# Kernel tuning notes

Measured on AMD Instinct MI355X. Metric: run time of the kernel, lower is better.

Reference implementation:

```python
import math
import jax, jax.numpy as jnp
import numpy as np

N_HEADS = 8

def setup_inputs() -> dict:
    key = jax.random.key(0)
    qkv = jax.random.normal(key, (4, 3 * N_HEADS * 64, 2048), dtype=jnp.float32)
    return {"qkv": qkv}

def reference(qkv) -> jnp.ndarray:
    bs, width, length = qkv.shape
    assert width % (3 * N_HEADS) == 0
    ch = width // (3 * N_HEADS)
    q, k, v = jnp.split(qkv, 3, axis=1)            # each [N, H*C, T]
    scale = 1.0 / math.sqrt(math.sqrt(ch))
    qh = (q * scale).reshape(bs * N_HEADS, ch, length)  # [BH, C, T]
    kh = (k * scale).reshape(bs * N_HEADS, ch, length)
    vh = v.reshape(bs * N_HEADS, ch, length)
    weight = jnp.einsum('bct,bcs->bts', qh, kh)    # [BH, T, T]
    weight = jax.nn.softmax(weight.astype(jnp.float32), axis=-1).astype(weight.dtype)
    a = jnp.einsum('bts,bcs->bct', weight, vh)     # [BH, C, T]
    return a.reshape(bs, -1, length)
```

## Files before the change

kernel.cpp:

```cpp
#include <hip/hip_runtime.h>
#include <math.h>

#define T_LEN 2048
#define CH 64
#define NH 8
#define STILE 64
#define TTILE 128
#define WT 32
#define NIT (T_LEN / STILE)
#define CSK 68
#define CS 72
#define QS 132

#define QSCALE 0.180336880972948929f

typedef __attribute__((ext_vector_type(4))) float  f32x4;
typedef __attribute__((ext_vector_type(8))) __bf16 bf16x8;
typedef __attribute__((ext_vector_type(4))) __bf16 bf16x4;

union SMem {
  float qstage[CH * QS];
  struct {
    __bf16 k_hi[2][STILE * CSK];
    __bf16 v_s [2][CH * CS];
    __bf16 p_s [4 * WT * CS];
  } loop;
};

#define MFMA(A, B, C) __builtin_amdgcn_mfma_f32_16x16x32_bf16((A), (B), (C), 0, 0, 0)

__device__ __forceinline__ void load_k(const float* kp, int s0, int tid, float2 (&kreg)[2][4]) {
#pragma unroll
  for (int rr = 0; rr < 2; ++rr) {
    int fidx = rr * 256 + tid;
    int cq  = fidx >> 5;
    int sp2 = fidx & 31;
    const float* kc = kp + (size_t)(4 * cq) * T_LEN + s0 + 2 * sp2;
#pragma unroll
    for (int r = 0; r < 4; ++r)
      kreg[rr][r] = *(const float2*)(kc + (size_t)r * T_LEN);
  }
}

__device__ __forceinline__ void store_k(__bf16* kh, int tid, const float2 (&kreg)[2][4]) {
#pragma unroll
  for (int rr = 0; rr < 2; ++rr) {
    int fidx = rr * 256 + tid;
    int cq  = fidx >> 5;
    int sp2 = fidx & 31;
    bf16x4 w0 = {(__bf16)kreg[rr][0].x, (__bf16)kreg[rr][1].x,
                 (__bf16)kreg[rr][2].x, (__bf16)kreg[rr][3].x};
    bf16x4 w1 = {(__bf16)kreg[rr][0].y, (__bf16)kreg[rr][1].y,
                 (__bf16)kreg[rr][2].y, (__bf16)kreg[rr][3].y};
    *(bf16x4*)&kh[(2 * sp2 + 0) * CSK + 4 * cq] = w0;
    *(bf16x4*)&kh[(2 * sp2 + 1) * CSK + 4 * cq] = w1;
  }
}

__device__ __forceinline__ void load_v(const float* vp, int s0, int tid, f32x4 (&vreg)[4]) {
#pragma unroll
  for (int rr = 0; rr < 4; ++rr) {
    int fidx = rr * 256 + tid;
    int c  = fidx >> 4;
    int s4 = (fidx & 15) << 2;
    vreg[rr] = *(const f32x4*)(vp + (size_t)c * T_LEN + s0 + s4);
  }
}

__device__ __forceinline__ void store_v(__bf16* vs, int tid, const f32x4 (&vreg)[4]) {
#pragma unroll
  for (int rr = 0; rr < 4; ++rr) {
    int fidx = rr * 256 + tid;
    int c  = fidx >> 4;
    int s4 = (fidx & 15) << 2;
    bf16x4 vv = {(__bf16)vreg[rr].x, (__bf16)vreg[rr].y,
                 (__bf16)vreg[rr].z, (__bf16)vreg[rr].w};
    *(bf16x4*)&vs[c * CS + s4] = vv;
  }
}

__global__ __launch_bounds__(256, 2)
void qkv_attn_mfma(const float* __restrict__ qkv, float* __restrict__ out) {
  __shared__ SMem sm;
  const int tid  = threadIdx.x;
  const int lane = tid & 63;
  const int wave = tid >> 6;
  const int tn   = lane & 15;
  const int quad = lane >> 4;

  const int ttile = blockIdx.x;
  const int bh    = blockIdx.y;
  const int b = bh >> 3, h = bh & 7;
  const size_t base = (size_t)b * (3 * NH * CH) * T_LEN;
  const float* qp = qkv + base + (size_t)(CH * h) * T_LEN;
  const float* kp = qkv + base + (size_t)(CH * (NH + h)) * T_LEN;
  const float* vp = qkv + base + (size_t)(CH * (2 * NH + h)) * T_LEN;
  const int t0 = ttile * TTILE;

#pragma unroll
  for (int rr = 0; rr < 8; ++rr) {
    int fidx = rr * 256 + tid;
    int c  = fidx >> 5;
    int t4 = (fidx & 31) << 2;
    f32x4 q4 = *(const f32x4*)(qp + (size_t)c * T_LEN + t0 + t4);
    *(f32x4*)&sm.qstage[c * QS + t4] = q4;
  }
  __syncthreads();

  bf16x8 qh[2][2], ql[2][2];
#pragma unroll
  for (int nb = 0; nb < 2; ++nb)
#pragma unroll
    for (int kb = 0; kb < 2; ++kb) {
      int tloc = wave * WT + nb * 16 + tn;
      bf16x8 H, L;
#pragma unroll
      for (int j = 0; j < 8; ++j) {
        float qv = sm.qstage[(kb * 32 + quad * 8 + j) * QS + tloc] * QSCALE;
        __bf16 hv = (__bf16)qv;
        H[j] = hv;
        L[j] = (__bf16)(qv - (float)hv);
      }
      qh[nb][kb] = H;
      ql[nb][kb] = L;
    }
  __syncthreads();

  f32x4 acc[4][2];
  float l_part[2] = {0.f, 0.f};
#pragma unroll
  for (int mb = 0; mb < 4; ++mb)
#pragma unroll
    for (int nb = 0; nb < 2; ++nb)
      acc[mb][nb] = (f32x4){0.f, 0.f, 0.f, 0.f};

  float2 kreg[2][4];
  f32x4  vreg[4];
  load_k(kp, 0, tid, kreg);
  load_v(vp, 0, tid, vreg);
  store_k(sm.loop.k_hi[0], tid, kreg);
  store_v(sm.loop.v_s[0], tid, vreg);
  __syncthreads();

  for (int it = 0; it < NIT; ++it) {
    const int cur = it & 1;
    const bool more = (it + 1 < NIT);
    const int snext = (it + 1) * STILE;

    if (more) {
      load_k(kp, snext, tid, kreg);
      load_v(vp, snext, tid, vreg);
    }

    const __bf16* kh = sm.loop.k_hi[cur];
    const __bf16* vs = sm.loop.v_s[cur];

    f32x4 d[4][2];
#pragma unroll
    for (int mb = 0; mb < 4; ++mb) {
      const int srow = (mb * 16 + tn) * CSK + quad * 8;
      bf16x4 a00 = *(const bf16x4*)&kh[srow];
      bf16x4 a01 = *(const bf16x4*)&kh[srow + 4];
      bf16x4 a10 = *(const bf16x4*)&kh[srow + 32];
      bf16x4 a11 = *(const bf16x4*)&kh[srow + 36];
      bf16x8 ah0 = __builtin_shufflevector(a00, a01, 0, 1, 2, 3, 4, 5, 6, 7);
      bf16x8 ah1 = __builtin_shufflevector(a10, a11, 0, 1, 2, 3, 4, 5, 6, 7);
#pragma unroll
      for (int nb = 0; nb < 2; ++nb) {
        f32x4 acc_d = (f32x4){0.f, 0.f, 0.f, 0.f};
        acc_d = MFMA(ah0, qh[nb][0], acc_d);
        acc_d = MFMA(ah0, ql[nb][0], acc_d);
        acc_d = MFMA(ah1, qh[nb][1], acc_d);
        acc_d = MFMA(ah1, ql[nb][1], acc_d);
        d[mb][nb] = acc_d;
      }
    }

#pragma unroll
    for (int nb = 0; nb < 2; ++nb) {
      float rs = 0.f;
#pragma unroll
      for (int mb = 0; mb < 4; ++mb)
#pragma unroll
        for (int r = 0; r < 4; ++r) {
          float e = __builtin_amdgcn_exp2f(d[mb][nb][r]);
          d[mb][nb][r] = e;
          rs += e;
        }
      l_part[nb] += rs;
    }

    bf16x8 av[4][2];
#pragma unroll
    for (int mb = 0; mb < 4; ++mb) {
      const int crow = (mb * 16 + tn) * CS + quad * 8;
      av[mb][0] = *(const bf16x8*)&vs[crow];
      av[mb][1] = *(const bf16x8*)&vs[crow + 32];
    }

    __bf16* pw = &sm.loop.p_s[wave * (WT * CS)];
#pragma unroll
    for (int nb = 0; nb < 2; ++nb)
#pragma unroll
      for (int mb = 0; mb < 4; ++mb) {
        f32x4 pv4 = d[mb][nb];
        bf16x4 pb = {(__bf16)pv4.x, (__bf16)pv4.y, (__bf16)pv4.z, (__bf16)pv4.w};
        *(bf16x4*)&pw[(nb * 16 + tn) * CS + mb * 16 + quad * 4] = pb;
      }

    asm volatile("" ::: "memory");

    bf16x8 bp[2][2];
#pragma unroll
    for (int nb = 0; nb < 2; ++nb)
#pragma unroll
      for (int kb = 0; kb < 2; ++kb)
        bp[nb][kb] = *(const bf16x8*)&pw[(nb * 16 + tn) * CS + kb * 32 + quad * 8];

#pragma unroll
    for (int mb = 0; mb < 4; ++mb)
#pragma unroll
      for (int nb = 0; nb < 2; ++nb) {
        acc[mb][nb] = MFMA(av[mb][0], bp[nb][0], acc[mb][nb]);
        acc[mb][nb] = MFMA(av[mb][1], bp[nb][1], acc[mb][nb]);
      }

    if (more) {
      store_k(sm.loop.k_hi[cur ^ 1], tid, kreg);
      store_v(sm.loop.v_s[cur ^ 1], tid, vreg);
    }
    __syncthreads();
  }

  float* op = out + (size_t)bh * CH * T_LEN;
#pragma unroll
  for (int nb = 0; nb < 2; ++nb) {
    float l = l_part[nb];
    l += __shfl_xor(l, 16, 64);
    l += __shfl_xor(l, 32, 64);
    float inv_l = 1.0f / l;
    int t = t0 + wave * WT + nb * 16 + tn;
#pragma unroll
    for (int mb = 0; mb < 4; ++mb) {
      f32x4 o = acc[mb][nb] * inv_l;
      int c = mb * 16 + quad * 4;
      op[(size_t)(c + 0) * T_LEN + t] = o.x;
      op[(size_t)(c + 1) * T_LEN + t] = o.y;
      op[(size_t)(c + 2) * T_LEN + t] = o.z;
      op[(size_t)(c + 3) * T_LEN + t] = o.w;
    }
  }
}

extern "C" void kernel_launch(void* const* d_in, const int* in_sizes, int n_in,
                              void* d_out, int out_size, void* d_ws, size_t ws_size,
                              hipStream_t stream) {
  const float* qkv = (const float*)d_in[0];
  float* out = (float*)d_out;
  dim3 grid(T_LEN / TTILE, 32);
  qkv_attn_mfma<<<grid, 256, 0, stream>>>(qkv, out);
}
```

Baseline: 133.9 us.

## Load V fragments directly from global into MFMA registers, drop V LDS staging

Each wave now reads its own V operand fragments straight from global memory in MFMA layout and converts them to bf16 in registers, instead of staging a shared V tile through LDS. This removes the LDS writes and reads for V and frees shared memory. The P stride is widened to cut bank conflicts. The trade-off is that all four waves redundantly load the same V tile from global/L2 each iteration, with no prefetch distance, which can expose load latency. QSCALE is also slightly changed.

```diff
diff --git a/kernel.cpp b/kernel.cpp
--- a/kernel.cpp
+++ b/kernel.cpp
@@ -9,10 +9,10 @@
 #define WT 32
 #define NIT (T_LEN / STILE)
 #define CSK 68
-#define CS 72
+#define PS 76
 #define QS 132
 
-#define QSCALE 0.180336880972948929f
+#define QSCALE 0.18033688011112043f
 
 typedef __attribute__((ext_vector_type(4))) float  f32x4;
 typedef __attribute__((ext_vector_type(8))) __bf16 bf16x8;
@@ -22,8 +22,7 @@
   float qstage[CH * QS];
   struct {
     __bf16 k_hi[2][STILE * CSK];
-    __bf16 v_s [2][CH * CS];
-    __bf16 p_s [4 * WT * CS];
+    __bf16 p_s [4 * WT * PS];
   } loop;
 };
 
@@ -57,28 +56,6 @@
   }
 }
 
-__device__ __forceinline__ void load_v(const float* vp, int s0, int tid, f32x4 (&vreg)[4]) {
-#pragma unroll
-  for (int rr = 0; rr < 4; ++rr) {
-    int fidx = rr * 256 + tid;
-    int c  = fidx >> 4;
-    int s4 = (fidx & 15) << 2;
-    vreg[rr] = *(const f32x4*)(vp + (size_t)c * T_LEN + s0 + s4);
-  }
-}
-
-__device__ __forceinline__ void store_v(__bf16* vs, int tid, const f32x4 (&vreg)[4]) {
-#pragma unroll
-  for (int rr = 0; rr < 4; ++rr) {
-    int fidx = rr * 256 + tid;
-    int c  = fidx >> 4;
-    int s4 = (fidx & 15) << 2;
-    bf16x4 vv = {(__bf16)vreg[rr].x, (__bf16)vreg[rr].y,
-                 (__bf16)vreg[rr].z, (__bf16)vreg[rr].w};
-    *(bf16x4*)&vs[c * CS + s4] = vv;
-  }
-}
-
 __global__ __launch_bounds__(256, 2)
 void qkv_attn_mfma(const float* __restrict__ qkv, float* __restrict__ out) {
   __shared__ SMem sm;
@@ -135,25 +112,31 @@
       acc[mb][nb] = (f32x4){0.f, 0.f, 0.f, 0.f};
 
   float2 kreg[2][4];
-  f32x4  vreg[4];
   load_k(kp, 0, tid, kreg);
-  load_v(vp, 0, tid, vreg);
   store_k(sm.loop.k_hi[0], tid, kreg);
-  store_v(sm.loop.v_s[0], tid, vreg);
   __syncthreads();
+
+  const float* vlane = vp + (size_t)tn * T_LEN + quad * 8;
 
   for (int it = 0; it < NIT; ++it) {
     const int cur = it & 1;
     const bool more = (it + 1 < NIT);
-    const int snext = (it + 1) * STILE;
-
-    if (more) {
-      load_k(kp, snext, tid, kreg);
-      load_v(vp, snext, tid, vreg);
+    const int s0 = it * STILE;
+
+    if (more) load_k(kp, s0 + STILE, tid, kreg);
+
+    f32x4 vf[4][2][2];
+#pragma unroll
+    for (int mb = 0; mb < 4; ++mb) {
+      const float* vr = vlane + (size_t)(16 * mb) * T_LEN + s0;
+#pragma unroll
+      for (int kb = 0; kb < 2; ++kb) {
+        vf[mb][kb][0] = *(const f32x4*)(vr + 32 * kb);
+        vf[mb][kb][1] = *(const f32x4*)(vr + 32 * kb + 4);
+      }
     }
 
     const __bf16* kh = sm.loop.k_hi[cur];
-    const __bf16* vs = sm.loop.v_s[cur];
 
     f32x4 d[4][2];
 #pragma unroll
@@ -190,22 +173,14 @@
       l_part[nb] += rs;
     }
 
-    bf16x8 av[4][2];
-#pragma unroll
-    for (int mb = 0; mb < 4; ++mb) {
-      const int crow = (mb * 16 + tn) * CS + quad * 8;
-      av[mb][0] = *(const bf16x8*)&vs[crow];
-      av[mb][1] = *(const bf16x8*)&vs[crow + 32];
-    }
-
-    __bf16* pw = &sm.loop.p_s[wave * (WT * CS)];
+    __bf16* pw = &sm.loop.p_s[wave * (WT * PS)];
 #pragma unroll
     for (int nb = 0; nb < 2; ++nb)
 #pragma unroll
       for (int mb = 0; mb < 4; ++mb) {
         f32x4 pv4 = d[mb][nb];
         bf16x4 pb = {(__bf16)pv4.x, (__bf16)pv4.y, (__bf16)pv4.z, (__bf16)pv4.w};
-        *(bf16x4*)&pw[(nb * 16 + tn) * CS + mb * 16 + quad * 4] = pb;
+        *(bf16x4*)&pw[(nb * 16 + tn) * PS + mb * 16 + quad * 4] = pb;
       }
 
     asm volatile("" ::: "memory");
@@ -215,20 +190,26 @@
     for (int nb = 0; nb < 2; ++nb)
 #pragma unroll
       for (int kb = 0; kb < 2; ++kb)
-        bp[nb][kb] = *(const bf16x8*)&pw[(nb * 16 + tn) * CS + kb * 32 + quad * 8];
-
-#pragma unroll
-    for (int mb = 0; mb < 4; ++mb)
+        bp[nb][kb] = *(const bf16x8*)&pw[(nb * 16 + tn) * PS + kb * 32 + quad * 8];
+
+#pragma unroll
+    for (int mb = 0; mb < 4; ++mb) {
+      bf16x8 av[2];
+#pragma unroll
+      for (int kb = 0; kb < 2; ++kb) {
+        f32x4 lo = vf[mb][kb][0], hi = vf[mb][kb][1];
+        bf16x8 a = {(__bf16)lo.x, (__bf16)lo.y, (__bf16)lo.z, (__bf16)lo.w,
+                    (__bf16)hi.x, (__bf16)hi.y, (__bf16)hi.z, (__bf16)hi.w};
+        av[kb] = a;
+      }
 #pragma unroll
       for (int nb = 0; nb < 2; ++nb) {
-        acc[mb][nb] = MFMA(av[mb][0], bp[nb][0], acc[mb][nb]);
-        acc[mb][nb] = MFMA(av[mb][1], bp[nb][1], acc[mb][nb]);
-      }
-
-    if (more) {
-      store_k(sm.loop.k_hi[cur ^ 1], tid, kreg);
-      store_v(sm.loop.v_s[cur ^ 1], tid, vreg);
-    }
+        acc[mb][nb] = MFMA(av[0], bp[nb][0], acc[mb][nb]);
+        acc[mb][nb] = MFMA(av[1], bp[nb][1], acc[mb][nb]);
+      }
+    }
+
+    if (more) store_k(sm.loop.k_hi[cur ^ 1], tid, kreg);
     __syncthreads();
   }
 
```

After: 218.6 us. 63.3% more time.

## Software-pipeline PV MFMA of previous tile with QK MFMA of current tile

Applied to the files above, without the earlier changes.

Restructures the main loop so the P·V matrix multiply for tile i-1 is issued in the same iteration as the Q·K multiply and exp for tile i. A prologue and an epilogue handle the first and last tiles, and the P and V fragments are carried across iterations. The goal is to let independent MFMA chains and the exp work interleave, hiding latency. The cost is more live registers for V fragments held across iterations, which could hurt occupancy at the 2-blocks-per-SM bound.

```diff
diff --git a/kernel.cpp b/kernel.cpp
--- a/kernel.cpp
+++ b/kernel.cpp
@@ -79,6 +79,90 @@
   }
 }
 
+__device__ __forceinline__ void read_kfrags(const __bf16* kh, int tn, int quad, bf16x8 (&ah)[4][2]) {
+#pragma unroll
+  for (int mb = 0; mb < 4; ++mb) {
+    const int srow = (mb * 16 + tn) * CSK + quad * 8;
+    bf16x4 a00 = *(const bf16x4*)&kh[srow];
+    bf16x4 a01 = *(const bf16x4*)&kh[srow + 4];
+    bf16x4 a10 = *(const bf16x4*)&kh[srow + 32];
+    bf16x4 a11 = *(const bf16x4*)&kh[srow + 36];
+    ah[mb][0] = __builtin_shufflevector(a00, a01, 0, 1, 2, 3, 4, 5, 6, 7);
+    ah[mb][1] = __builtin_shufflevector(a10, a11, 0, 1, 2, 3, 4, 5, 6, 7);
+  }
+}
+
+__device__ __forceinline__ void read_vfrags(const __bf16* vs, int tn, int quad, bf16x8 (&av)[4][2]) {
+#pragma unroll
+  for (int mb = 0; mb < 4; ++mb) {
+    const int crow = (mb * 16 + tn) * CS + quad * 8;
+    av[mb][0] = *(const bf16x8*)&vs[crow];
+    av[mb][1] = *(const bf16x8*)&vs[crow + 32];
+  }
+}
+
+__device__ __forceinline__ void read_pfrags(const __bf16* pw, int tn, int quad, bf16x8 (&bp)[2][2]) {
+#pragma unroll
+  for (int nb = 0; nb < 2; ++nb)
+#pragma unroll
+    for (int kb = 0; kb < 2; ++kb)
+      bp[nb][kb] = *(const bf16x8*)&pw[(nb * 16 + tn) * CS + kb * 32 + quad * 8];
+}
+
+__device__ __forceinline__ void qk_mfma(const bf16x8 (&ah)[4][2],
+                                        const bf16x8 (&qh)[2][2], const bf16x8 (&ql)[2][2],
+                                        f32x4 (&d)[4][2]) {
+#pragma unroll
+  for (int mb = 0; mb < 4; ++mb)
+#pragma unroll
+    for (int nb = 0; nb < 2; ++nb) {
+      f32x4 t = (f32x4){0.f, 0.f, 0.f, 0.f};
+      t = MFMA(ah[mb][0], qh[nb][0], t);
+      t = MFMA(ah[mb][0], ql[nb][0], t);
+      t = MFMA(ah[mb][1], qh[nb][1], t);
+      t = MFMA(ah[mb][1], ql[nb][1], t);
+      d[mb][nb] = t;
+    }
+}
+
+__device__ __forceinline__ void pv_mfma(const bf16x8 (&av)[4][2], const bf16x8 (&bp)[2][2],
+                                        f32x4 (&acc)[4][2]) {
+#pragma unroll
+  for (int mb = 0; mb < 4; ++mb)
+#pragma unroll
+    for (int nb = 0; nb < 2; ++nb) {
+      acc[mb][nb] = MFMA(av[mb][0], bp[nb][0], acc[mb][nb]);
+      acc[mb][nb] = MFMA(av[mb][1], bp[nb][1], acc[mb][nb]);
+    }
+}
+
+__device__ __forceinline__ void softmax_exp(f32x4 (&d)[4][2], float (&l_part)[2]) {
+#pragma unroll
+  for (int nb = 0; nb < 2; ++nb) {
+    float rs = 0.f;
+#pragma unroll
+    for (int mb = 0; mb < 4; ++mb)
+#pragma unroll
+      for (int r = 0; r < 4; ++r) {
+        float e = __builtin_amdgcn_exp2f(d[mb][nb][r]);
+        d[mb][nb][r] = e;
+        rs += e;
+      }
+    l_part[nb] += rs;
+  }
+}
+
+__device__ __forceinline__ void write_p(__bf16* pw, int tn, int quad, const f32x4 (&d)[4][2]) {
+#pragma unroll
+  for (int nb = 0; nb < 2; ++nb)
+#pragma unroll
+    for (int mb = 0; mb < 4; ++mb) {
+      f32x4 pv4 = d[mb][nb];
+      bf16x4 pb = {(__bf16)pv4.x, (__bf16)pv4.y, (__bf16)pv4.z, (__bf16)pv4.w};
+      *(bf16x4*)&pw[(nb * 16 + tn) * CS + mb * 16 + quad * 4] = pb;
+    }
+}
+
 __global__ __launch_bounds__(256, 2)
 void qkv_attn_mfma(const float* __restrict__ qkv, float* __restrict__ out) {
   __shared__ SMem sm;
@@ -134,6 +218,8 @@
     for (int nb = 0; nb < 2; ++nb)
       acc[mb][nb] = (f32x4){0.f, 0.f, 0.f, 0.f};
 
+  __bf16* pw = &sm.loop.p_s[wave * (WT * CS)];
+
   float2 kreg[2][4];
   f32x4  vreg[4];
   load_k(kp, 0, tid, kreg);
@@ -142,94 +228,57 @@
   store_v(sm.loop.v_s[0], tid, vreg);
   __syncthreads();
 
-  for (int it = 0; it < NIT; ++it) {
+  bf16x8 av[4][2];
+
+  {
+    bf16x8 ah[4][2];
+    read_kfrags(sm.loop.k_hi[0], tn, quad, ah);
+    load_k(kp, STILE, tid, kreg);
+    load_v(vp, STILE, tid, vreg);
+    f32x4 d[4][2];
+    qk_mfma(ah, qh, ql, d);
+    softmax_exp(d, l_part);
+    write_p(pw, tn, quad, d);
+    read_vfrags(sm.loop.v_s[0], tn, quad, av);
+    store_k(sm.loop.k_hi[1], tid, kreg);
+    store_v(sm.loop.v_s[1], tid, vreg);
+    __syncthreads();
+  }
+
+  for (int it = 1; it < NIT; ++it) {
     const int cur = it & 1;
     const bool more = (it + 1 < NIT);
-    const int snext = (it + 1) * STILE;
+
+    bf16x8 bp[2][2];
+    read_pfrags(pw, tn, quad, bp);
+    bf16x8 ah[4][2];
+    read_kfrags(sm.loop.k_hi[cur], tn, quad, ah);
 
     if (more) {
-      load_k(kp, snext, tid, kreg);
-      load_v(vp, snext, tid, vreg);
-    }
-
-    const __bf16* kh = sm.loop.k_hi[cur];
-    const __bf16* vs = sm.loop.v_s[cur];
-
+      load_k(kp, (it + 1) * STILE, tid, kreg);
+      load_v(vp, (it + 1) * STILE, tid, vreg);
+    }
+
+    pv_mfma(av, bp, acc);
     f32x4 d[4][2];
-#pragma unroll
-    for (int mb = 0; mb < 4; ++mb) {
-      const int srow = (mb * 16 + tn) * CSK + quad * 8;
-      bf16x4 a00 = *(const bf16x4*)&kh[srow];
-      bf16x4 a01 = *(const bf16x4*)&kh[srow + 4];
-      bf16x4 a10 = *(const bf16x4*)&kh[srow + 32];
-      bf16x4 a11 = *(const bf16x4*)&kh[srow + 36];
-      bf16x8 ah0 = __builtin_shufflevector(a00, a01, 0, 1, 2, 3, 4, 5, 6, 7);
-      bf16x8 ah1 = __builtin_shufflevector(a10, a11, 0, 1, 2, 3, 4, 5, 6, 7);
-#pragma unroll
-      for (int nb = 0; nb < 2; ++nb) {
-        f32x4 acc_d = (f32x4){0.f, 0.f, 0.f, 0.f};
-        acc_d = MFMA(ah0, qh[nb][0], acc_d);
-        acc_d = MFMA(ah0, ql[nb][0], acc_d);
-        acc_d = MFMA(ah1, qh[nb][1], acc_d);
-        acc_d = MFMA(ah1, ql[nb][1], acc_d);
-        d[mb][nb] = acc_d;
-      }
-    }
-
-#pragma unroll
-    for (int nb = 0; nb < 2; ++nb) {
-      float rs = 0.f;
-#pragma unroll
-      for (int mb = 0; mb < 4; ++mb)
-#pragma unroll
-        for (int r = 0; r < 4; ++r) {
-          float e = __builtin_amdgcn_exp2f(d[mb][nb][r]);
-          d[mb][nb][r] = e;
-          rs += e;
-        }
-      l_part[nb] += rs;
-    }
-
-    bf16x8 av[4][2];
-#pragma unroll
-    for (int mb = 0; mb < 4; ++mb) {
-      const int crow = (mb * 16 + tn) * CS + quad * 8;
-      av[mb][0] = *(const bf16x8*)&vs[crow];
-      av[mb][1] = *(const bf16x8*)&vs[crow + 32];
-    }
-
-    __bf16* pw = &sm.loop.p_s[wave * (WT * CS)];
-#pragma unroll
-    for (int nb = 0; nb < 2; ++nb)
-#pragma unroll
-      for (int mb = 0; mb < 4; ++mb) {
-        f32x4 pv4 = d[mb][nb];
-        bf16x4 pb = {(__bf16)pv4.x, (__bf16)pv4.y, (__bf16)pv4.z, (__bf16)pv4.w};
-        *(bf16x4*)&pw[(nb * 16 + tn) * CS + mb * 16 + quad * 4] = pb;
-      }
+    qk_mfma(ah, qh, ql, d);
+    softmax_exp(d, l_part);
 
     asm volatile("" ::: "memory");
-
-    bf16x8 bp[2][2];
-#pragma unroll
-    for (int nb = 0; nb < 2; ++nb)
-#pragma unroll
-      for (int kb = 0; kb < 2; ++kb)
-        bp[nb][kb] = *(const bf16x8*)&pw[(nb * 16 + tn) * CS + kb * 32 + quad * 8];
-
-#pragma unroll
-    for (int mb = 0; mb < 4; ++mb)
-#pragma unroll
-      for (int nb = 0; nb < 2; ++nb) {
-        acc[mb][nb] = MFMA(av[mb][0], bp[nb][0], acc[mb][nb]);
-        acc[mb][nb] = MFMA(av[mb][1], bp[nb][1], acc[mb][nb]);
-      }
+    write_p(pw, tn, quad, d);
+    read_vfrags(sm.loop.v_s[cur], tn, quad, av);
 
     if (more) {
       store_k(sm.loop.k_hi[cur ^ 1], tid, kreg);
       store_v(sm.loop.v_s[cur ^ 1], tid, vreg);
     }
     __syncthreads();
+  }
+
+  {
+    bf16x8 bp[2][2];
+    read_pfrags(pw, tn, quad, bp);
+    pv_mfma(av, bp, acc);
   }
 
   float* op = out + (size_t)bh * CH * T_LEN;
```

Measured after the change: 136.2 us. No clear change (+1.7%).

## Split key dimension across wave pairs, drop Q low-part MFMAs, software-pipeline PV

Applied to the files above, without the earlier changes.

Doubles the block to 512 threads so two wave groups each handle half of every 64-wide key tile, then merges their partial outputs and row sums through shared memory at the end. The Q hi/lo split-bf16 correction is removed, halving QK MFMAs at some cost in precision. The PV product is deferred one iteration using a triple-buffered V tile so it overlaps with the next QK step. Together these aim to cut per-wave serial work and raise occupancy, at the cost of a shared-memory reduction and lower score accuracy.

```diff
diff --git a/kernel.cpp b/kernel.cpp
--- a/kernel.cpp
+++ b/kernel.cpp
@@ -10,7 +10,9 @@
 #define NIT (T_LEN / STILE)
 #define CSK 68
 #define CS 72
+#define PS2 40
 #define QS 132
+#define RS 68
 
 #define QSCALE 0.180336880972948929f
 
@@ -22,55 +24,49 @@
   float qstage[CH * QS];
   struct {
     __bf16 k_hi[2][STILE * CSK];
-    __bf16 v_s [2][CH * CS];
-    __bf16 p_s [4 * WT * CS];
+    __bf16 v_s [3][CH * CS];
+    __bf16 p_s [8 * WT * PS2];
   } loop;
+  struct {
+    float o[4][WT][RS];
+    float l[4][2][4][16];
+  } red;
 };
 
 #define MFMA(A, B, C) __builtin_amdgcn_mfma_f32_16x16x32_bf16((A), (B), (C), 0, 0, 0)
 
-__device__ __forceinline__ void load_k(const float* kp, int s0, int tid, float2 (&kreg)[2][4]) {
+__device__ __forceinline__ void load_k(const float* kp, int s0, int tid, float2 (&kreg)[4]) {
+  int cq  = tid >> 5;
+  int sp2 = tid & 31;
+  const float* kc = kp + (size_t)(4 * cq) * T_LEN + s0 + 2 * sp2;
+#pragma unroll
+  for (int r = 0; r < 4; ++r)
+    kreg[r] = *(const float2*)(kc + (size_t)r * T_LEN);
+}
+
+__device__ __forceinline__ void store_k(__bf16* kh, int tid, const float2 (&kreg)[4]) {
+  int cq  = tid >> 5;
+  int sp2 = tid & 31;
+  bf16x4 w0 = {(__bf16)kreg[0].x, (__bf16)kreg[1].x, (__bf16)kreg[2].x, (__bf16)kreg[3].x};
+  bf16x4 w1 = {(__bf16)kreg[0].y, (__bf16)kreg[1].y, (__bf16)kreg[2].y, (__bf16)kreg[3].y};
+  *(bf16x4*)&kh[(2 * sp2 + 0) * CSK + 4 * cq] = w0;
+  *(bf16x4*)&kh[(2 * sp2 + 1) * CSK + 4 * cq] = w1;
+}
+
+__device__ __forceinline__ void load_v(const float* vp, int s0, int tid, f32x4 (&vreg)[2]) {
 #pragma unroll
   for (int rr = 0; rr < 2; ++rr) {
-    int fidx = rr * 256 + tid;
-    int cq  = fidx >> 5;
-    int sp2 = fidx & 31;
-    const float* kc = kp + (size_t)(4 * cq) * T_LEN + s0 + 2 * sp2;
-#pragma unroll
-    for (int r = 0; r < 4; ++r)
-      kreg[rr][r] = *(const float2*)(kc + (size_t)r * T_LEN);
-  }
-}
-
-__device__ __forceinline__ void store_k(__bf16* kh, int tid, const float2 (&kreg)[2][4]) {
-#pragma unroll
-  for (int rr = 0; rr < 2; ++rr) {
-    int fidx = rr * 256 + tid;
-    int cq  = fidx >> 5;
-    int sp2 = fidx & 31;
-    bf16x4 w0 = {(__bf16)kreg[rr][0].x, (__bf16)kreg[rr][1].x,
-                 (__bf16)kreg[rr][2].x, (__bf16)kreg[rr][3].x};
-    bf16x4 w1 = {(__bf16)kreg[rr][0].y, (__bf16)kreg[rr][1].y,
-                 (__bf16)kreg[rr][2].y, (__bf16)kreg[rr][3].y};
-    *(bf16x4*)&kh[(2 * sp2 + 0) * CSK + 4 * cq] = w0;
-    *(bf16x4*)&kh[(2 * sp2 + 1) * CSK + 4 * cq] = w1;
-  }
-}
-
-__device__ __forceinline__ void load_v(const float* vp, int s0, int tid, f32x4 (&vreg)[4]) {
-#pragma unroll
-  for (int rr = 0; rr < 4; ++rr) {
-    int fidx = rr * 256 + tid;
+    int fidx = rr * 512 + tid;
     int c  = fidx >> 4;
     int s4 = (fidx & 15) << 2;
     vreg[rr] = *(const f32x4*)(vp + (size_t)c * T_LEN + s0 + s4);
   }
 }
 
-__device__ __forceinline__ void store_v(__bf16* vs, int tid, const f32x4 (&vreg)[4]) {
-#pragma unroll
-  for (int rr = 0; rr < 4; ++rr) {
-    int fidx = rr * 256 + tid;
+__device__ __forceinline__ void store_v(__bf16* vs, int tid, const f32x4 (&vreg)[2]) {
+#pragma unroll
+  for (int rr = 0; rr < 2; ++rr) {
+    int fidx = rr * 512 + tid;
     int c  = fidx >> 4;
     int s4 = (fidx & 15) << 2;
     bf16x4 vv = {(__bf16)vreg[rr].x, (__bf16)vreg[rr].y,
@@ -79,12 +75,14 @@
   }
 }
 
-__global__ __launch_bounds__(256, 2)
+__global__ __launch_bounds__(512, 4)
 void qkv_attn_mfma(const float* __restrict__ qkv, float* __restrict__ out) {
   __shared__ SMem sm;
   const int tid  = threadIdx.x;
   const int lane = tid & 63;
   const int wave = tid >> 6;
+  const int wt   = wave & 3;
+  const int ws   = wave >> 2;
   const int tn   = lane & 15;
   const int quad = lane >> 4;
 
@@ -98,8 +96,8 @@
   const int t0 = ttile * TTILE;
 
 #pragma unroll
-  for (int rr = 0; rr < 8; ++rr) {
-    int fidx = rr * 256 + tid;
+  for (int rr = 0; rr < 4; ++rr) {
+    int fidx = rr * 512 + tid;
     int c  = fidx >> 5;
     int t4 = (fidx & 31) << 2;
     f32x4 q4 = *(const f32x4*)(qp + (size_t)c * T_LEN + t0 + t4);
@@ -107,80 +105,96 @@
   }
   __syncthreads();
 
-  bf16x8 qh[2][2], ql[2][2];
+  bf16x8 qh[2][2];
 #pragma unroll
   for (int nb = 0; nb < 2; ++nb)
 #pragma unroll
     for (int kb = 0; kb < 2; ++kb) {
-      int tloc = wave * WT + nb * 16 + tn;
-      bf16x8 H, L;
+      int tloc = wt * WT + nb * 16 + tn;
+      bf16x8 H;
 #pragma unroll
       for (int j = 0; j < 8; ++j) {
         float qv = sm.qstage[(kb * 32 + quad * 8 + j) * QS + tloc] * QSCALE;
-        __bf16 hv = (__bf16)qv;
-        H[j] = hv;
-        L[j] = (__bf16)(qv - (float)hv);
+        H[j] = (__bf16)qv;
       }
       qh[nb][kb] = H;
-      ql[nb][kb] = L;
     }
   __syncthreads();
 
   f32x4 acc[4][2];
   float l_part[2] = {0.f, 0.f};
 #pragma unroll
-  for (int mb = 0; mb < 4; ++mb)
+  for (int mbc = 0; mbc < 4; ++mbc)
 #pragma unroll
     for (int nb = 0; nb < 2; ++nb)
-      acc[mb][nb] = (f32x4){0.f, 0.f, 0.f, 0.f};
-
-  float2 kreg[2][4];
-  f32x4  vreg[4];
+      acc[mbc][nb] = (f32x4){0.f, 0.f, 0.f, 0.f};
+
+  __bf16* pw = &sm.loop.p_s[wave * (WT * PS2)];
+
+  float2 kreg[4];
+  f32x4  vreg[2];
   load_k(kp, 0, tid, kreg);
   load_v(vp, 0, tid, vreg);
   store_k(sm.loop.k_hi[0], tid, kreg);
   store_v(sm.loop.v_s[0], tid, vreg);
   __syncthreads();
 
+  int vrd = 2, vwr = 1;
+
   for (int it = 0; it < NIT; ++it) {
-    const int cur = it & 1;
+    const int kcur = it & 1;
     const bool more = (it + 1 < NIT);
-    const int snext = (it + 1) * STILE;
+
+    if (it > 0) {
+      bf16x8 bp[2];
+#pragma unroll
+      for (int nb = 0; nb < 2; ++nb)
+        bp[nb] = *(const bf16x8*)&pw[(nb * 16 + tn) * PS2 + quad * 8];
+      bf16x8 av[4];
+      const __bf16* vs = sm.loop.v_s[vrd];
+#pragma unroll
+      for (int mbc = 0; mbc < 4; ++mbc)
+        av[mbc] = *(const bf16x8*)&vs[(16 * mbc + tn) * CS + 32 * ws + quad * 8];
+#pragma unroll
+      for (int mbc = 0; mbc < 4; ++mbc)
+#pragma unroll
+        for (int nb = 0; nb < 2; ++nb)
+          acc[mbc][nb] = MFMA(av[mbc], bp[nb], acc[mbc][nb]);
+    }
 
     if (more) {
-      load_k(kp, snext, tid, kreg);
-      load_v(vp, snext, tid, vreg);
-    }
-
-    const __bf16* kh = sm.loop.k_hi[cur];
-    const __bf16* vs = sm.loop.v_s[cur];
-
-    f32x4 d[4][2];
-#pragma unroll
-    for (int mb = 0; mb < 4; ++mb) {
-      const int srow = (mb * 16 + tn) * CSK + quad * 8;
-      bf16x4 a00 = *(const bf16x4*)&kh[srow];
-      bf16x4 a01 = *(const bf16x4*)&kh[srow + 4];
-      bf16x4 a10 = *(const bf16x4*)&kh[srow + 32];
-      bf16x4 a11 = *(const bf16x4*)&kh[srow + 36];
-      bf16x8 ah0 = __builtin_shufflevector(a00, a01, 0, 1, 2, 3, 4, 5, 6, 7);
-      bf16x8 ah1 = __builtin_shufflevector(a10, a11, 0, 1, 2, 3, 4, 5, 6, 7);
+      load_k(kp, (it + 1) * STILE, tid, kreg);
+      load_v(vp, (it + 1) * STILE, tid, vreg);
+    }
+
+    const __bf16* kh = sm.loop.k_hi[kcur];
+    bf16x8 ah[2][2];
+#pragma unroll
+    for (int mb = 0; mb < 2; ++mb) {
+      const int srow = (32 * ws + 16 * mb + tn) * CSK;
+#pragma unroll
+      for (int kb = 0; kb < 2; ++kb) {
+        bf16x4 a0 = *(const bf16x4*)&kh[srow + 32 * kb + quad * 8];
+        bf16x4 a1 = *(const bf16x4*)&kh[srow + 32 * kb + quad * 8 + 4];
+        ah[mb][kb] = __builtin_shufflevector(a0, a1, 0, 1, 2, 3, 4, 5, 6, 7);
+      }
+    }
+    f32x4 d[2][2];
+#pragma unroll
+    for (int mb = 0; mb < 2; ++mb)
 #pragma unroll
       for (int nb = 0; nb < 2; ++nb) {
-        f32x4 acc_d = (f32x4){0.f, 0.f, 0.f, 0.f};
-        acc_d = MFMA(ah0, qh[nb][0], acc_d);
-        acc_d = MFMA(ah0, ql[nb][0], acc_d);
-        acc_d = MFMA(ah1, qh[nb][1], acc_d);
-        acc_d = MFMA(ah1, ql[nb][1], acc_d);
-        d[mb][nb] = acc_d;
-      }
-    }
+        f32x4 t = (f32x4){0.f, 0.f, 0.f, 0.f};
+        t = MFMA(ah[mb][0], qh[nb][0], t);
+        t = MFMA(ah[mb][1], qh[nb][1], t);
+        d[mb][nb] = t;
+      }
 
 #pragma unroll
     for (int nb = 0; nb < 2; ++nb) {
       float rs = 0.f;
 #pragma unroll
-      for (int mb = 0; mb < 4; ++mb)
+      for (int mb = 0; mb < 2; ++mb)
 #pragma unroll
         for (int r = 0; r < 4; ++r) {
           float e = __builtin_amdgcn_exp2f(d[mb][nb][r]);
@@ -190,64 +204,73 @@
       l_part[nb] += rs;
     }
 
-    bf16x8 av[4][2];
-#pragma unroll
-    for (int mb = 0; mb < 4; ++mb) {
-      const int crow = (mb * 16 + tn) * CS + quad * 8;
-      av[mb][0] = *(const bf16x8*)&vs[crow];
-      av[mb][1] = *(const bf16x8*)&vs[crow + 32];
-    }
-
-    __bf16* pw = &sm.loop.p_s[wave * (WT * CS)];
+    asm volatile("" ::: "memory");
+
 #pragma unroll
     for (int nb = 0; nb < 2; ++nb)
 #pragma unroll
-      for (int mb = 0; mb < 4; ++mb) {
+      for (int mb = 0; mb < 2; ++mb) {
         f32x4 pv4 = d[mb][nb];
         bf16x4 pb = {(__bf16)pv4.x, (__bf16)pv4.y, (__bf16)pv4.z, (__bf16)pv4.w};
-        *(bf16x4*)&pw[(nb * 16 + tn) * CS + mb * 16 + quad * 4] = pb;
-      }
-
-    asm volatile("" ::: "memory");
-
-    bf16x8 bp[2][2];
+        *(bf16x4*)&pw[(nb * 16 + tn) * PS2 + mb * 16 + quad * 4] = pb;
+      }
+
+    if (more) {
+      store_k(sm.loop.k_hi[kcur ^ 1], tid, kreg);
+      store_v(sm.loop.v_s[vwr], tid, vreg);
+    }
+    vrd = (vrd == 2) ? 0 : vrd + 1;
+    vwr = (vwr == 2) ? 0 : vwr + 1;
+    __syncthreads();
+  }
+
+  {
+    bf16x8 bp[2];
 #pragma unroll
     for (int nb = 0; nb < 2; ++nb)
-#pragma unroll
-      for (int kb = 0; kb < 2; ++kb)
-        bp[nb][kb] = *(const bf16x8*)&pw[(nb * 16 + tn) * CS + kb * 32 + quad * 8];
-
-#pragma unroll
-    for (int mb = 0; mb < 4; ++mb)
-#pragma unroll
-      for (int nb = 0; nb < 2; ++nb) {
-        acc[mb][nb] = MFMA(av[mb][0], bp[nb][0], acc[mb][nb]);
-        acc[mb][nb] = MFMA(av[mb][1], bp[nb][1], acc[mb][nb]);
-      }
-
-    if (more) {
-      store_k(sm.loop.k_hi[cur ^ 1], tid, kreg);
-      store_v(sm.loop.v_s[cur ^ 1], tid, vreg);
-    }
-    __syncthreads();
-  }
-
-  float* op = out + (size_t)bh * CH * T_LEN;
-#pragma unroll
-  for (int nb = 0; nb < 2; ++nb) {
-    float l = l_part[nb];
-    l += __shfl_xor(l, 16, 64);
-    l += __shfl_xor(l, 32, 64);
-    float inv_l = 1.0f / l;
-    int t = t0 + wave * WT + nb * 16 + tn;
-#pragma unroll
-    for (int mb = 0; mb < 4; ++mb) {
-      f32x4 o = acc[mb][nb] * inv_l;
-      int c = mb * 16 + quad * 4;
-      op[(size_t)(c + 0) * T_LEN + t] = o.x;
-      op[(size_t)(c + 1) * T_LEN + t] = o.y;
-      op[(size_t)(c + 2) * T_LEN + t] = o.z;
-      op[(size_t)(c + 3) * T_LEN + t] = o.w;
+      bp[nb] = *(const bf16x8*)&pw[(nb * 16 + tn) * PS2 + quad * 8];
+    bf16x8 av[4];
+    const __bf16* vs = sm.loop.v_s[vrd];
+#pragma unroll
+    for (int mbc = 0; mbc < 4; ++mbc)
+      av[mbc] = *(const bf16x8*)&vs[(16 * mbc + tn) * CS + 32 * ws + quad * 8];
+#pragma unroll
+    for (int mbc = 0; mbc < 4; ++mbc)
+#pragma unroll
+      for (int nb = 0; nb < 2; ++nb)
+        acc[mbc][nb] = MFMA(av[mbc], bp[nb], acc[mbc][nb]);
+  }
+  __syncthreads();
+
+  if (ws == 1) {
+#pragma unroll
+    for (int nb = 0; nb < 2; ++nb) {
+      sm.red.l[wt][nb][quad][tn] = l_part[nb];
+#pragma unroll
+      for (int mbc = 0; mbc < 4; ++mbc)
+        *(f32x4*)&sm.red.o[wt][nb * 16 + tn][16 * mbc + quad * 4] = acc[mbc][nb];
+    }
+  }
+  __syncthreads();
+  if (ws == 0) {
+    float* op = out + (size_t)bh * CH * T_LEN;
+#pragma unroll
+    for (int nb = 0; nb < 2; ++nb) {
+      float l = l_part[nb] + sm.red.l[wt][nb][quad][tn];
+      l += __shfl_xor(l, 16, 64);
+      l += __shfl_xor(l, 32, 64);
+      float inv_l = 1.0f / l;
+      int t = t0 + wt * WT + nb * 16 + tn;
+#pragma unroll
+      for (int mbc = 0; mbc < 4; ++mbc) {
+        f32x4 o = acc[mbc][nb] + *(const f32x4*)&sm.red.o[wt][nb * 16 + tn][16 * mbc + quad * 4];
+        o = o * inv_l;
+        int c = 16 * mbc + quad * 4;
+        op[(size_t)(c + 0) * T_LEN + t] = o.x;
+        op[(size_t)(c + 1) * T_LEN + t] = o.y;
+        op[(size_t)(c + 2) * T_LEN + t] = o.z;
+        op[(size_t)(c + 3) * T_LEN + t] = o.w;
+      }
     }
   }
 }
@@ -258,5 +281,5 @@
   const float* qkv = (const float*)d_in[0];
   float* out = (float*)d_out;
   dim3 grid(T_LEN / TTILE, 32);
-  qkv_attn_mfma<<<grid, 256, 0, stream>>>(qkv, out);
-}
+  qkv_attn_mfma<<<grid, 512, 0, stream>>>(qkv, out);
+}
```

New measurement: 129.3 us. 1.04x faster.
